# Optimization experiments

Hardware: AMD Instinct MI355X
Metric: run time of the kernel (lower is better)

The kernel has to match this reference:

```python
import jax, jax.numpy as jnp
import numpy as np

INIT_RANGE = 0.02

def setup_inputs() -> dict:
    key = jax.random.key(0)
    ks = jax.random.split(key, 5)
    B, S, D, H, Dh = 4, 2048, 768, 12, 64
    residual = jax.random.normal(ks[0], (B, S, D), dtype=jnp.float32)
    W_Q = jax.random.normal(ks[1], (H, D, Dh), dtype=jnp.float32) * INIT_RANGE
    W_K = jax.random.normal(ks[2], (H, D, Dh), dtype=jnp.float32) * INIT_RANGE
    W_V = jax.random.normal(ks[3], (H, D, Dh), dtype=jnp.float32) * INIT_RANGE
    W_O = jax.random.normal(ks[4], (H, Dh, D), dtype=jnp.float32) * INIT_RANGE
    b_Q = jnp.zeros((H, Dh), dtype=jnp.float32)
    b_K = jnp.zeros((H, Dh), dtype=jnp.float32)
    b_V = jnp.zeros((H, Dh), dtype=jnp.float32)
    b_O = jnp.zeros((D,), dtype=jnp.float32)
    return {"residual": residual, "W_Q": W_Q, "W_K": W_K, "W_V": W_V,
            "W_O": W_O, "b_Q": b_Q, "b_K": b_K, "b_V": b_V, "b_O": b_O}

def reference(residual, W_Q, W_K, W_V, W_O, b_Q, b_K, b_V, b_O):
    # residual: [b, s, d]; W_{Q,K,V}: [h, d, dh]; W_O: [h, dh, d]
    d_head = W_Q.shape[-1]
    q = jnp.einsum('bsd,hde->bshe', residual, W_Q) + b_Q  # [b, s, h, dh]
    k = jnp.einsum('bsd,hde->bshe', residual, W_K) + b_K
    v = jnp.einsum('bsd,hde->bshe', residual, W_V) + b_V
    scores = jnp.einsum('bqhe,bkhe->bhqk', q, k) / jnp.sqrt(jnp.float32(d_head))
    S = residual.shape[1]
    causal = jnp.tril(jnp.ones((S, S), dtype=bool))  # True where attending allowed
    scores = jnp.where(causal, scores, -jnp.inf)
    pattern = jax.nn.softmax(scores, axis=-1)  # [b, h, q, k]
    z = jnp.einsum('bkhe,bhqk->bqhe', v, pattern)  # [b, q, h, dh]
    attn_out = jnp.einsum('bqhe,hed->bqd', z, W_O) + b_O
    return attn_out
```

## Files before the change

kernel.cpp:

```cpp
#include <hip/hip_runtime.h>

typedef short short8 __attribute__((ext_vector_type(8)));
typedef float floatx4 __attribute__((ext_vector_type(4)));
typedef unsigned short ushort_t;


__device__ inline ushort_t f2bf(float f) {
  union { float f; unsigned u; } x; x.f = f;
  unsigned u = x.u;
  unsigned r = u + 0x7fffu + ((u >> 16) & 1u);
  return (ushort_t)(r >> 16);
}

__device__ inline unsigned pk2(float a, float b) {
  union { float f; unsigned u; } x, y; x.f = a; y.f = b;
  return ((x.u + 0x8000u) >> 16) | ((y.u + 0x8000u) & 0xffff0000u);
}

__device__ inline float fexp2(float x) {
#if __has_builtin(__builtin_amdgcn_exp2f)
  return __builtin_amdgcn_exp2f(x);
#else
  return exp2f(x);
#endif
}

__device__ inline void async16(const void* g, void* l) {
  __builtin_amdgcn_global_load_lds((const __attribute__((address_space(1))) void*)g,
                                   (__attribute__((address_space(3))) void*)l,
                                   16, 0, 0);
}


__global__ __launch_bounds__(256) void conv_prep(
    const float* __restrict__ x, ushort_t* __restrict__ rx,
    const float* __restrict__ wq, const float* __restrict__ wk, const float* __restrict__ wv,
    const float* __restrict__ wo,
    const float* __restrict__ bq, const float* __restrict__ bk, const float* __restrict__ bv,
    ushort_t* __restrict__ wqkvT, ushort_t* __restrict__ woT, float* __restrict__ bqkv)
{
  __shared__ ushort_t t[64 * 72];
  const int tid = threadIdx.x;
  const int bid0 = blockIdx.x;
  if (bid0 < 6144) {
    int i = bid0 * 256 + tid;
    float4 f = ((const float4*)x)[i];
    ushort4 o;
    o.x = f2bf(f.x); o.y = f2bf(f.y); o.z = f2bf(f.z); o.w = f2bf(f.w);
    ((ushort4*)rx)[i] = o;
    return;
  }
  const int bid = bid0 - 6144;
  if (bid < 432) {
    int m = bid / 144, rem = bid % 144;
    int h = rem / 12, dt = rem % 12;
    int d0 = dt * 64;
    const float* w = (m == 0) ? wq : ((m == 1) ? wk : wv);
    const float* src = w + ((size_t)h * 768 + d0) * 64;
#pragma unroll
    for (int i = 0; i < 4; ++i) {
      int task = i * 256 + tid;
      int row = task >> 4, c4 = task & 15;
      float4 f = *(const float4*)(src + row * 64 + c4 * 4);
      ushort4 o4;
      o4.x = f2bf(f.x); o4.y = f2bf(f.y); o4.z = f2bf(f.z); o4.w = f2bf(f.w);
      *(ushort4*)&t[row * 72 + c4 * 4] = o4;
    }
    __syncthreads();
    ushort_t* dst = wqkvT + ((size_t)m * 768 + h * 64) * 768 + d0;
#pragma unroll
    for (int i = 0; i < 2; ++i) {
      int task = i * 256 + tid;
      int e = task >> 3, sc = task & 7;
      short8 d8;
#pragma unroll
      for (int j = 0; j < 8; ++j) d8[j] = (short)t[(sc * 8 + j) * 72 + e];
      *(short8*)(dst + (size_t)e * 768 + sc * 8) = d8;
    }
  } else if (bid < 576) {
    int b2 = bid - 432;
    int het = b2 / 12, dt = b2 % 12;
    int he0 = het * 64, d0 = dt * 64;
    const float* src = wo + (size_t)he0 * 768 + d0;
#pragma unroll
    for (int i = 0; i < 4; ++i) {
      int task = i * 256 + tid;
      int row = task >> 4, c4 = task & 15;
      float4 f = *(const float4*)(src + (size_t)row * 768 + c4 * 4);
      ushort4 o4;
      o4.x = f2bf(f.x); o4.y = f2bf(f.y); o4.z = f2bf(f.z); o4.w = f2bf(f.w);
      *(ushort4*)&t[row * 72 + c4 * 4] = o4;
    }
    __syncthreads();
    ushort_t* dst = woT + (size_t)d0 * 768 + he0;
#pragma unroll
    for (int i = 0; i < 2; ++i) {
      int task = i * 256 + tid;
      int dd = task >> 3, sc = task & 7;
      short8 d8;
#pragma unroll
      for (int j = 0; j < 8; ++j) d8[j] = (short)t[(sc * 8 + j) * 72 + dd];
      *(short8*)(dst + (size_t)dd * 768 + sc * 8) = d8;
    }
  } else {
    for (int idx = tid; idx < 2304; idx += 256) {
      int m = idx / 768, rem = idx - m * 768;
      const float* bp = (m == 0) ? bq : ((m == 1) ? bk : bv);
      bqkv[idx] = bp[rem];
    }
  }
}


__global__ __launch_bounds__(256) void gemm_qkv(
    const ushort_t* __restrict__ A, const ushort_t* __restrict__ Bt,
    const float* __restrict__ bias,
    ushort_t* __restrict__ q, ushort_t* __restrict__ k, ushort_t* __restrict__ vt)
{
  __shared__ ushort_t sh[17408];
  const int tid = threadIdx.x;
  const int wave = tid >> 6, lane = tid & 63;
  const int ln15 = lane & 15, quad = lane >> 4;
  const int id = blockIdx.x;
  const int xk = id & 7, j = id >> 3;
  const int bx = (xk >> 1) * 16 + (j & 15);
  const int by = (xk & 1) * 9 + (j >> 4);
  const int row0 = bx * 128, col0 = by * 128;
  const int wm = (wave >> 1) * 64, wn = (wave & 1) * 64;
  const int c0 = wave * 2;

  const ushort_t* gA0 = A + (size_t)(row0 + c0 * 16 + (lane >> 2)) * 768 + (lane & 3) * 8;
  const ushort_t* gB0 = Bt + (size_t)(col0 + c0 * 16 + (lane >> 2)) * 768 + (lane & 3) * 8;

  floatx4 acc[4][4];
#pragma unroll
  for (int mi = 0; mi < 4; ++mi)
#pragma unroll
    for (int ni = 0; ni < 4; ++ni)
      acc[mi][ni] = (floatx4){0.f, 0.f, 0.f, 0.f};

  async16(gA0, &sh[c0 * 512]);
  async16(gA0 + 16 * 768, &sh[c0 * 512 + 512]);
  async16(gB0, &sh[8192 + c0 * 512]);
  async16(gB0 + 16 * 768, &sh[8192 + c0 * 512 + 512]);
  __syncthreads();

  for (int kt = 0; kt < 24; ++kt) {
    const int buf = kt & 1;
    if (kt + 1 < 24) {
      ushort_t* dA = &sh[(buf ^ 1) * 4096];
      ushort_t* dB = &sh[8192 + (buf ^ 1) * 4096];
      async16(gA0 + (kt + 1) * 32, dA + c0 * 512);
      async16(gA0 + (kt + 1) * 32 + 16 * 768, dA + c0 * 512 + 512);
      async16(gB0 + (kt + 1) * 32, dB + c0 * 512);
      async16(gB0 + (kt + 1) * 32 + 16 * 768, dB + c0 * 512 + 512);
    }
    const ushort_t* sA = &sh[buf * 4096];
    const ushort_t* sB = &sh[8192 + buf * 4096];
    short8 af[4], bfv[4];
#pragma unroll
    for (int mi = 0; mi < 4; ++mi)
      af[mi] = *(const short8*)&sA[(wm + mi * 16 + ln15) * 32 + quad * 8];
#pragma unroll
    for (int ni = 0; ni < 4; ++ni)
      bfv[ni] = *(const short8*)&sB[(wn + ni * 16 + ln15) * 32 + quad * 8];
#pragma unroll
    for (int mi = 0; mi < 4; ++mi)
#pragma unroll
      for (int ni = 0; ni < 4; ++ni)
        acc[mi][ni] = __builtin_amdgcn_mfma_f32_16x16x32_bf16(af[mi], bfv[ni], acc[mi][ni], 0, 0, 0);
    __syncthreads();
  }

  if (col0 < 1536) {
    const float qscale = 0.125f * 1.44269504f;
#pragma unroll
    for (int mi = 0; mi < 4; ++mi) {
#pragma unroll
      for (int ni = 0; ni < 4; ++ni) {
        int gr = row0 + wm + mi * 16 + quad * 4;
        int gc = col0 + wn + ni * 16 + ln15;
        float bia = bias[gc];
        int m = gc >> 9 >> 1;
        m = gc / 768;
        int rem = gc - m * 768;
        int h = rem >> 6, e = rem & 63;
        ushort_t* dp = (m == 0) ? q : k;
#pragma unroll
        for (int r = 0; r < 4; ++r) {
          float val = acc[mi][ni][r] + bia;
          int rr = gr + r;
          int bb = rr >> 11, ss = rr & 2047;
          size_t dst = ((size_t)((bb * 12 + h) * 2048 + ss) << 6) + e;
          dp[dst] = f2bf((m == 0) ? val * qscale : val);
        }
      }
    }
  } else {
#pragma unroll
    for (int mi = 0; mi < 4; ++mi) {
#pragma unroll
      for (int ni = 0; ni < 4; ++ni) {
        int col = wn + ni * 16 + ln15;
        int rowb = wm + mi * 16 + quad * 4;
        float bia = bias[col0 + col];
        ushort4 w4;
        w4.x = f2bf(acc[mi][ni][0] + bia);
        w4.y = f2bf(acc[mi][ni][1] + bia);
        w4.z = f2bf(acc[mi][ni][2] + bia);
        w4.w = f2bf(acc[mi][ni][3] + bia);
        *(ushort4*)&sh[col * 136 + rowb] = w4;
      }
    }
    __syncthreads();
    const int relc0 = col0 - 1536;
    const int bb = row0 >> 11, s0 = row0 & 2047;
#pragma unroll
    for (int i = 0; i < 8; ++i) {
      int g = i * 256 + tid;
      int col = g >> 4, chunk = g & 15;
      short8 d = *(const short8*)&sh[col * 136 + chunk * 8];
      int hh = (relc0 + col) >> 6;
      int ee = col & 63;
      *(short8*)(vt + (((size_t)(bb * 12 + hh) * 64 + ee) << 11) + s0 + chunk * 8) = d;
    }
  }
}


__global__ __launch_bounds__(256) void gemm_out(
    const ushort_t* __restrict__ A, const ushort_t* __restrict__ Bt,
    const float* __restrict__ bias, float* __restrict__ outf)
{
  __shared__ ushort_t lA[2][64 * 32];
  __shared__ ushort_t lB[2][128 * 32];
  const int tid = threadIdx.x;
  const int wave = tid >> 6, lane = tid & 63;
  const int ln15 = lane & 15, quad = lane >> 4;
  const int id = blockIdx.x;
  const int xk = id & 7, j = id >> 3;
  const int bx = xk * 16 + (j & 15);
  const int by = j >> 4;
  const int row0 = bx * 64, col0 = by * 128;
  const int wm = (wave >> 1) * 32, wn = (wave & 1) * 64;
  const int cb = wave * 2;

  const ushort_t* gA0 = A + (size_t)(row0 + wave * 16 + (lane >> 2)) * 768 + (lane & 3) * 8;
  const ushort_t* gB0 = Bt + (size_t)(col0 + cb * 16 + (lane >> 2)) * 768 + (lane & 3) * 8;

  floatx4 acc[2][4];
#pragma unroll
  for (int mi = 0; mi < 2; ++mi)
#pragma unroll
    for (int ni = 0; ni < 4; ++ni)
      acc[mi][ni] = (floatx4){0.f, 0.f, 0.f, 0.f};

  async16(gA0, &lA[0][wave * 512]);
  async16(gB0, &lB[0][cb * 512]);
  async16(gB0 + 16 * 768, &lB[0][cb * 512 + 512]);
  __syncthreads();

  for (int kt = 0; kt < 24; ++kt) {
    const int buf = kt & 1;
    if (kt + 1 < 24) {
      async16(gA0 + (kt + 1) * 32, &lA[buf ^ 1][wave * 512]);
      async16(gB0 + (kt + 1) * 32, &lB[buf ^ 1][cb * 512]);
      async16(gB0 + (kt + 1) * 32 + 16 * 768, &lB[buf ^ 1][cb * 512 + 512]);
    }
    short8 af[2], bfv[4];
#pragma unroll
    for (int mi = 0; mi < 2; ++mi)
      af[mi] = *(const short8*)&lA[buf][(wm + mi * 16 + ln15) * 32 + quad * 8];
#pragma unroll
    for (int ni = 0; ni < 4; ++ni)
      bfv[ni] = *(const short8*)&lB[buf][(wn + ni * 16 + ln15) * 32 + quad * 8];
#pragma unroll
    for (int mi = 0; mi < 2; ++mi)
#pragma unroll
      for (int ni = 0; ni < 4; ++ni)
        acc[mi][ni] = __builtin_amdgcn_mfma_f32_16x16x32_bf16(af[mi], bfv[ni], acc[mi][ni], 0, 0, 0);
    __syncthreads();
  }

#pragma unroll
  for (int mi = 0; mi < 2; ++mi) {
#pragma unroll
    for (int ni = 0; ni < 4; ++ni) {
      int gr = row0 + wm + mi * 16 + quad * 4;
      int gc = col0 + wn + ni * 16 + ln15;
      float bia = bias[gc];
#pragma unroll
      for (int r = 0; r < 4; ++r)
        outf[(size_t)(gr + r) * 768 + gc] = acc[mi][ni][r] + bia;
    }
  }
}


__device__ inline short8 frag_ld(const ushort_t* t, int row, int ch) {
  return *(const short8*)&t[row * 64 + (((ch ^ row) & 7) * 8)];
}

__global__ __launch_bounds__(256) void attn3(
    const ushort_t* __restrict__ Q, const ushort_t* __restrict__ K,
    const ushort_t* __restrict__ VT, ushort_t* __restrict__ Z)
{
  __shared__ ushort_t lK[2][64 * 64];
  __shared__ ushort_t lV[2][64 * 64];
  __shared__ ushort_t lPQ[128 * 64];
  const int tid = threadIdx.x;
  const int wave = tid >> 6, lane = tid & 63;
  const int ln15 = lane & 15, quad = lane >> 4;
  const int bi = blockIdx.x;
  const int bh = bi % 48;
  const int t = 15 - (bi / 48);
  const int h = bh % 12, b = bh / 12;
  const size_t base = (size_t)bh * 2048 * 64;
  const ushort_t* Qp = Q + base + (size_t)t * 128 * 64;
  const ushort_t* Kp = K + base;
  const ushort_t* Vp = VT + base;
  const int nk = 2 * t + 2;

  const int srow = tid >> 3, slch = tid & 7;
  const int sc_ = slch ^ (srow & 7);

#pragma unroll
  for (int i = 0; i < 4; ++i) {
    int task = i * 256 + tid;
    int row = task >> 3;
    int c = slch ^ (row & 7);
    async16(Qp + row * 64 + c * 8, &lPQ[task * 8]);
  }
  async16(Kp + (size_t)srow * 64 + sc_ * 8, &lK[0][tid * 8]);
  async16(Kp + (size_t)(srow + 32) * 64 + sc_ * 8, &lK[0][(256 + tid) * 8]);
  async16(Vp + (size_t)srow * 2048 + sc_ * 8, &lV[0][tid * 8]);
  async16(Vp + (size_t)(srow + 32) * 2048 + sc_ * 8, &lV[0][(256 + tid) * 8]);

  const ushort_t* kPre0 = Kp + (size_t)(64 + srow) * 64 + sc_ * 8;
  const ushort_t* kPre1 = kPre0 + 32 * 64;
  const ushort_t* vPre0 = Vp + (size_t)srow * 2048 + 64 + sc_ * 8;
  const ushort_t* vPre1 = vPre0 + 32 * 2048;

  __syncthreads();
  short8 qf[2][2];
#pragma unroll
  for (int c = 0; c < 2; ++c) {
    qf[c][0] = frag_ld(lPQ, wave * 32 + c * 16 + ln15, quad);
    qf[c][1] = frag_ld(lPQ, wave * 32 + c * 16 + ln15, quad + 4);
  }
  __syncthreads();

  float l_i[2] = {0.f, 0.f};
  floatx4 o[2][4];
#pragma unroll
  for (int c = 0; c < 2; ++c)
#pragma unroll
    for (int et = 0; et < 4; ++et) o[c][et] = (floatx4){0.f, 0.f, 0.f, 0.f};

  ushort_t* lPw = lPQ + wave * 2048;
  const int qg0 = t * 128 + wave * 32 + ln15;

  for (int kt = 0; kt < nk; ++kt) {
    const int buf = kt & 1;
    if (kt + 1 < nk) {
      ushort_t* dK = lK[buf ^ 1];
      ushort_t* dV = lV[buf ^ 1];
      async16(kPre0, dK + tid * 8);
      async16(kPre1, dK + (256 + tid) * 8);
      async16(vPre0, dV + tid * 8);
      async16(vPre1, dV + (256 + tid) * 8);
      kPre0 += 4096; kPre1 += 4096; vPre0 += 64; vPre1 += 64;
    }

    floatx4 st[2][4];
#pragma unroll
    for (int ni = 0; ni < 4; ++ni) {
      short8 kf0 = frag_ld(lK[buf], ni * 16 + ln15, quad);
      short8 kf1 = frag_ld(lK[buf], ni * 16 + ln15, quad + 4);
#pragma unroll
      for (int c = 0; c < 2; ++c) {
        floatx4 z4 = (floatx4){0.f, 0.f, 0.f, 0.f};
        z4 = __builtin_amdgcn_mfma_f32_16x16x32_bf16(kf0, qf[c][0], z4, 0, 0, 0);
        st[c][ni] = __builtin_amdgcn_mfma_f32_16x16x32_bf16(kf1, qf[c][1], z4, 0, 0, 0);
      }
    }

    const bool masked = (kt >= 2 * t);
#pragma unroll
    for (int c = 0; c < 2; ++c) {
      const int qg = qg0 + c * 16;
      float p[16];
      float rs = 0.f;
#pragma unroll
      for (int ni = 0; ni < 4; ++ni)
#pragma unroll
        for (int r = 0; r < 4; ++r) {
          float x = st[c][ni][r];
          if (masked) {
            int kg = kt * 64 + ni * 16 + quad * 4 + r;
            x = (kg <= qg) ? x : -1e30f;
          }
          float pe = fexp2(x);
          p[ni * 4 + r] = pe;
          rs += pe;
        }
      rs += __shfl_xor(rs, 16);
      rs += __shfl_xor(rs, 32);
      l_i[c] += rs;
      const int rowl = c * 16 + ln15;
#pragma unroll
      for (int ni = 0; ni < 4; ++ni) {
        int chunk = 2 * ni + (quad >> 1);
        int pos = chunk ^ (rowl & 7);
        uint2 w;
        w.x = pk2(p[ni * 4 + 0], p[ni * 4 + 1]);
        w.y = pk2(p[ni * 4 + 2], p[ni * 4 + 3]);
        *(uint2*)&lPw[rowl * 64 + pos * 8 + (quad & 1) * 4] = w;
      }
    }

    short8 pf[2][2];
#pragma unroll
    for (int c = 0; c < 2; ++c) {
      pf[c][0] = frag_ld(lPw, c * 16 + ln15, quad);
      pf[c][1] = frag_ld(lPw, c * 16 + ln15, quad + 4);
    }
#pragma unroll
    for (int et = 0; et < 4; ++et) {
      short8 vf0 = frag_ld(lV[buf], et * 16 + ln15, quad);
      short8 vf1 = frag_ld(lV[buf], et * 16 + ln15, quad + 4);
#pragma unroll
      for (int c = 0; c < 2; ++c) {
        o[c][et] = __builtin_amdgcn_mfma_f32_16x16x32_bf16(vf0, pf[c][0], o[c][et], 0, 0, 0);
        o[c][et] = __builtin_amdgcn_mfma_f32_16x16x32_bf16(vf1, pf[c][1], o[c][et], 0, 0, 0);
      }
    }
    __syncthreads();
  }

#pragma unroll
  for (int c = 0; c < 2; ++c) {
    float inv = 1.f / l_i[c];
    size_t zrow = (size_t)(b * 2048 + t * 128 + wave * 32 + c * 16 + ln15);
#pragma unroll
    for (int et = 0; et < 4; ++et) {
      ushort4 w;
      w.x = f2bf(o[c][et][0] * inv);
      w.y = f2bf(o[c][et][1] * inv);
      w.z = f2bf(o[c][et][2] * inv);
      w.w = f2bf(o[c][et][3] * inv);
      *(ushort4*)&Z[zrow * 768 + h * 64 + et * 16 + quad * 4] = w;
    }
  }
}


extern "C" void kernel_launch(void* const* d_in, const int* in_sizes, int n_in,
                              void* d_out, int out_size, void* d_ws, size_t ws_size,
                              hipStream_t stream)
{
  const float* residual = (const float*)d_in[0];
  const float* W_Q = (const float*)d_in[1];
  const float* W_K = (const float*)d_in[2];
  const float* W_V = (const float*)d_in[3];
  const float* W_O = (const float*)d_in[4];
  const float* b_Q = (const float*)d_in[5];
  const float* b_K = (const float*)d_in[6];
  const float* b_V = (const float*)d_in[7];
  const float* b_O = (const float*)d_in[8];
  float* out = (float*)d_out;

  char* w = (char*)d_ws;
  ushort_t* rx    = (ushort_t*)(w + 0);
  ushort_t* wqkvT = (ushort_t*)(w + 12582912);
  ushort_t* woT   = (ushort_t*)(w + 16121856);
  float*    bqkv  = (float*)   (w + 17301504);
  ushort_t* q     = (ushort_t*)(w + 17310720);
  ushort_t* k     = (ushort_t*)(w + 29893632);
  ushort_t* vt    = (ushort_t*)(w + 55059456);
  ushort_t* z     = rx;

  conv_prep<<<6721, 256, 0, stream>>>(residual, rx, W_Q, W_K, W_V, W_O,
                                      b_Q, b_K, b_V, wqkvT, woT, bqkv);
  gemm_qkv<<<1152, 256, 0, stream>>>(rx, wqkvT, bqkv, q, k, vt);
  attn3<<<768, 256, 0, stream>>>(q, k, vt, z);
  gemm_out<<<768, 256, 0, stream>>>(z, woT, b_O, out);
}
```

Measured before the change: 220.0 us.

## Vectorize GEMM epilogues, shrink QKV LDS, skip fully-masked attention tiles

Swaps the MFMA operand order in the Q/K part of the QKV GEMM and in the output GEMM, so each lane holds four consecutive columns and can write them as ushort4 or float4, with the bias read as float4. The V transpose goes through LDS in two 64-column halves, which cuts LDS to 32 KB, and a launch-bounds hint of 5 blocks is added to raise occupancy. In attention, waves 0-1 skip the last KV tile, which lies fully above the causal diagonal for their rows. pk2 now uses a byte-permute builtin. These target scattered scalar stores, LDS-limited occupancy and wasted masked work, at the cost of an extra barrier in the V path and possible register pressure from the occupancy hint.

New measurement: 359.2 us. 1.63x slower.

```diff
diff --git a/kernel.cpp b/kernel.cpp
--- a/kernel.cpp
+++ b/kernel.cpp
@@ -14,7 +14,7 @@
 
 __device__ inline unsigned pk2(float a, float b) {
   union { float f; unsigned u; } x, y; x.f = a; y.f = b;
-  return ((x.u + 0x8000u) >> 16) | ((y.u + 0x8000u) & 0xffff0000u);
+  return __builtin_amdgcn_perm(y.u + 0x8000u, x.u + 0x8000u, 0x07060302u);
 }
 
 __device__ inline float fexp2(float x) {
@@ -112,12 +112,12 @@
 }
 
 
-__global__ __launch_bounds__(256) void gemm_qkv(
+__global__ __launch_bounds__(256, 5) void gemm_qkv(
     const ushort_t* __restrict__ A, const ushort_t* __restrict__ Bt,
     const float* __restrict__ bias,
     ushort_t* __restrict__ q, ushort_t* __restrict__ k, ushort_t* __restrict__ vt)
 {
-  __shared__ ushort_t sh[17408];
+  __shared__ ushort_t sh[16384];
   const int tid = threadIdx.x;
   const int wave = tid >> 6, lane = tid & 63;
   const int ln15 = lane & 15, quad = lane >> 4;
@@ -128,6 +128,7 @@
   const int row0 = bx * 128, col0 = by * 128;
   const int wm = (wave >> 1) * 64, wn = (wave & 1) * 64;
   const int c0 = wave * 2;
+  const bool is_v = (col0 >= 1536);
 
   const ushort_t* gA0 = A + (size_t)(row0 + c0 * 16 + (lane >> 2)) * 768 + (lane & 3) * 8;
   const ushort_t* gB0 = Bt + (size_t)(col0 + c0 * 16 + (lane >> 2)) * 768 + (lane & 3) * 8;
@@ -145,84 +146,115 @@
   async16(gB0 + 16 * 768, &sh[8192 + c0 * 512 + 512]);
   __syncthreads();
 
-  for (int kt = 0; kt < 24; ++kt) {
-    const int buf = kt & 1;
-    if (kt + 1 < 24) {
-      ushort_t* dA = &sh[(buf ^ 1) * 4096];
-      ushort_t* dB = &sh[8192 + (buf ^ 1) * 4096];
-      async16(gA0 + (kt + 1) * 32, dA + c0 * 512);
-      async16(gA0 + (kt + 1) * 32 + 16 * 768, dA + c0 * 512 + 512);
-      async16(gB0 + (kt + 1) * 32, dB + c0 * 512);
-      async16(gB0 + (kt + 1) * 32 + 16 * 768, dB + c0 * 512 + 512);
-    }
-    const ushort_t* sA = &sh[buf * 4096];
-    const ushort_t* sB = &sh[8192 + buf * 4096];
-    short8 af[4], bfv[4];
-#pragma unroll
-    for (int mi = 0; mi < 4; ++mi)
-      af[mi] = *(const short8*)&sA[(wm + mi * 16 + ln15) * 32 + quad * 8];
-#pragma unroll
-    for (int ni = 0; ni < 4; ++ni)
-      bfv[ni] = *(const short8*)&sB[(wn + ni * 16 + ln15) * 32 + quad * 8];
-#pragma unroll
-    for (int mi = 0; mi < 4; ++mi)
+  if (!is_v) {
+    for (int kt = 0; kt < 24; ++kt) {
+      const int buf = kt & 1;
+      if (kt + 1 < 24) {
+        ushort_t* dA = &sh[(buf ^ 1) * 4096];
+        ushort_t* dB = &sh[8192 + (buf ^ 1) * 4096];
+        async16(gA0 + (kt + 1) * 32, dA + c0 * 512);
+        async16(gA0 + (kt + 1) * 32 + 16 * 768, dA + c0 * 512 + 512);
+        async16(gB0 + (kt + 1) * 32, dB + c0 * 512);
+        async16(gB0 + (kt + 1) * 32 + 16 * 768, dB + c0 * 512 + 512);
+      }
+      const ushort_t* sA = &sh[buf * 4096];
+      const ushort_t* sB = &sh[8192 + buf * 4096];
+      short8 af[4], bfv[4];
+#pragma unroll
+      for (int mi = 0; mi < 4; ++mi)
+        af[mi] = *(const short8*)&sA[(wm + mi * 16 + ln15) * 32 + quad * 8];
 #pragma unroll
       for (int ni = 0; ni < 4; ++ni)
-        acc[mi][ni] = __builtin_amdgcn_mfma_f32_16x16x32_bf16(af[mi], bfv[ni], acc[mi][ni], 0, 0, 0);
-    __syncthreads();
-  }
-
-  if (col0 < 1536) {
+        bfv[ni] = *(const short8*)&sB[(wn + ni * 16 + ln15) * 32 + quad * 8];
+#pragma unroll
+      for (int mi = 0; mi < 4; ++mi)
+#pragma unroll
+        for (int ni = 0; ni < 4; ++ni)
+          acc[mi][ni] = __builtin_amdgcn_mfma_f32_16x16x32_bf16(bfv[ni], af[mi], acc[mi][ni], 0, 0, 0);
+      __syncthreads();
+    }
     const float qscale = 0.125f * 1.44269504f;
 #pragma unroll
     for (int mi = 0; mi < 4; ++mi) {
+      int rr = row0 + wm + mi * 16 + ln15;
+      int bb = rr >> 11, ss = rr & 2047;
 #pragma unroll
       for (int ni = 0; ni < 4; ++ni) {
-        int gr = row0 + wm + mi * 16 + quad * 4;
-        int gc = col0 + wn + ni * 16 + ln15;
-        float bia = bias[gc];
-        int m = gc >> 9 >> 1;
-        m = gc / 768;
-        int rem = gc - m * 768;
-        int h = rem >> 6, e = rem & 63;
-        ushort_t* dp = (m == 0) ? q : k;
-#pragma unroll
-        for (int r = 0; r < 4; ++r) {
-          float val = acc[mi][ni][r] + bia;
-          int rr = gr + r;
-          int bb = rr >> 11, ss = rr & 2047;
-          size_t dst = ((size_t)((bb * 12 + h) * 2048 + ss) << 6) + e;
-          dp[dst] = f2bf((m == 0) ? val * qscale : val);
-        }
+        int gc0 = col0 + wn + ni * 16 + quad * 4;
+        int m = (gc0 >= 768) ? 1 : 0;
+        int rem = gc0 - m * 768;
+        int h = rem >> 6, e0 = rem & 63;
+        float4 b4 = *(const float4*)&bias[gc0];
+        float sc = m ? 1.f : qscale;
+        ushort_t* dp = m ? k : q;
+        ushort4 w4;
+        w4.x = f2bf((acc[mi][ni][0] + b4.x) * sc);
+        w4.y = f2bf((acc[mi][ni][1] + b4.y) * sc);
+        w4.z = f2bf((acc[mi][ni][2] + b4.z) * sc);
+        w4.w = f2bf((acc[mi][ni][3] + b4.w) * sc);
+        *(ushort4*)(dp + (((size_t)(bb * 12 + h) * 2048 + ss) << 6) + e0) = w4;
       }
     }
   } else {
-#pragma unroll
-    for (int mi = 0; mi < 4; ++mi) {
-#pragma unroll
-      for (int ni = 0; ni < 4; ++ni) {
-        int col = wn + ni * 16 + ln15;
-        int rowb = wm + mi * 16 + quad * 4;
-        float bia = bias[col0 + col];
-        ushort4 w4;
-        w4.x = f2bf(acc[mi][ni][0] + bia);
-        w4.y = f2bf(acc[mi][ni][1] + bia);
-        w4.z = f2bf(acc[mi][ni][2] + bia);
-        w4.w = f2bf(acc[mi][ni][3] + bia);
-        *(ushort4*)&sh[col * 136 + rowb] = w4;
-      }
-    }
-    __syncthreads();
+    for (int kt = 0; kt < 24; ++kt) {
+      const int buf = kt & 1;
+      if (kt + 1 < 24) {
+        ushort_t* dA = &sh[(buf ^ 1) * 4096];
+        ushort_t* dB = &sh[8192 + (buf ^ 1) * 4096];
+        async16(gA0 + (kt + 1) * 32, dA + c0 * 512);
+        async16(gA0 + (kt + 1) * 32 + 16 * 768, dA + c0 * 512 + 512);
+        async16(gB0 + (kt + 1) * 32, dB + c0 * 512);
+        async16(gB0 + (kt + 1) * 32 + 16 * 768, dB + c0 * 512 + 512);
+      }
+      const ushort_t* sA = &sh[buf * 4096];
+      const ushort_t* sB = &sh[8192 + buf * 4096];
+      short8 af[4], bfv[4];
+#pragma unroll
+      for (int mi = 0; mi < 4; ++mi)
+        af[mi] = *(const short8*)&sA[(wm + mi * 16 + ln15) * 32 + quad * 8];
+#pragma unroll
+      for (int ni = 0; ni < 4; ++ni)
+        bfv[ni] = *(const short8*)&sB[(wn + ni * 16 + ln15) * 32 + quad * 8];
+#pragma unroll
+      for (int mi = 0; mi < 4; ++mi)
+#pragma unroll
+        for (int ni = 0; ni < 4; ++ni)
+          acc[mi][ni] = __builtin_amdgcn_mfma_f32_16x16x32_bf16(af[mi], bfv[ni], acc[mi][ni], 0, 0, 0);
+      __syncthreads();
+    }
     const int relc0 = col0 - 1536;
     const int bb = row0 >> 11, s0 = row0 & 2047;
-#pragma unroll
-    for (int i = 0; i < 8; ++i) {
-      int g = i * 256 + tid;
-      int col = g >> 4, chunk = g & 15;
-      short8 d = *(const short8*)&sh[col * 136 + chunk * 8];
-      int hh = (relc0 + col) >> 6;
-      int ee = col & 63;
-      *(short8*)(vt + (((size_t)(bb * 12 + hh) * 64 + ee) << 11) + s0 + chunk * 8) = d;
+    const int myhalf = wn >> 6;
+#pragma unroll
+    for (int hf = 0; hf < 2; ++hf) {
+      if (myhalf == hf) {
+#pragma unroll
+        for (int mi = 0; mi < 4; ++mi) {
+#pragma unroll
+          for (int ni = 0; ni < 4; ++ni) {
+            int col = wn + ni * 16 + ln15;
+            int rowb = wm + mi * 16 + quad * 4;
+            float bia = bias[col0 + col];
+            ushort4 w4;
+            w4.x = f2bf(acc[mi][ni][0] + bia);
+            w4.y = f2bf(acc[mi][ni][1] + bia);
+            w4.z = f2bf(acc[mi][ni][2] + bia);
+            w4.w = f2bf(acc[mi][ni][3] + bia);
+            *(ushort4*)&sh[(col & 63) * 136 + rowb] = w4;
+          }
+        }
+      }
+      __syncthreads();
+#pragma unroll
+      for (int i = 0; i < 4; ++i) {
+        int g = i * 256 + tid;
+        int lc = g >> 4, chunk = g & 15;
+        short8 d = *(const short8*)&sh[lc * 136 + chunk * 8];
+        int c = hf * 64 + lc;
+        int hh = (relc0 + c) >> 6, ee = (relc0 + c) & 63;
+        *(short8*)(vt + (((size_t)(bb * 12 + hh) * 64 + ee) << 11) + s0 + chunk * 8) = d;
+      }
+      if (hf == 0) __syncthreads();
     }
   }
 }
@@ -278,20 +310,23 @@
     for (int mi = 0; mi < 2; ++mi)
 #pragma unroll
       for (int ni = 0; ni < 4; ++ni)
-        acc[mi][ni] = __builtin_amdgcn_mfma_f32_16x16x32_bf16(af[mi], bfv[ni], acc[mi][ni], 0, 0, 0);
+        acc[mi][ni] = __builtin_amdgcn_mfma_f32_16x16x32_bf16(bfv[ni], af[mi], acc[mi][ni], 0, 0, 0);
     __syncthreads();
   }
 
 #pragma unroll
   for (int mi = 0; mi < 2; ++mi) {
+    int gr = row0 + wm + mi * 16 + ln15;
 #pragma unroll
     for (int ni = 0; ni < 4; ++ni) {
-      int gr = row0 + wm + mi * 16 + quad * 4;
-      int gc = col0 + wn + ni * 16 + ln15;
-      float bia = bias[gc];
-#pragma unroll
-      for (int r = 0; r < 4; ++r)
-        outf[(size_t)(gr + r) * 768 + gc] = acc[mi][ni][r] + bia;
+      int gc0 = col0 + wn + ni * 16 + quad * 4;
+      float4 b4 = *(const float4*)&bias[gc0];
+      float4 w4;
+      w4.x = acc[mi][ni][0] + b4.x;
+      w4.y = acc[mi][ni][1] + b4.y;
+      w4.z = acc[mi][ni][2] + b4.z;
+      w4.w = acc[mi][ni][3] + b4.w;
+      *(float4*)&outf[(size_t)gr * 768 + gc0] = w4;
     }
   }
 }
@@ -372,67 +407,70 @@
       kPre0 += 4096; kPre1 += 4096; vPre0 += 64; vPre1 += 64;
     }
 
-    floatx4 st[2][4];
-#pragma unroll
-    for (int ni = 0; ni < 4; ++ni) {
-      short8 kf0 = frag_ld(lK[buf], ni * 16 + ln15, quad);
-      short8 kf1 = frag_ld(lK[buf], ni * 16 + ln15, quad + 4);
+    const bool skip = (kt == nk - 1) && (wave < 2);
+    if (!skip) {
+      floatx4 st[2][4];
+#pragma unroll
+      for (int ni = 0; ni < 4; ++ni) {
+        short8 kf0 = frag_ld(lK[buf], ni * 16 + ln15, quad);
+        short8 kf1 = frag_ld(lK[buf], ni * 16 + ln15, quad + 4);
+#pragma unroll
+        for (int c = 0; c < 2; ++c) {
+          floatx4 z4 = (floatx4){0.f, 0.f, 0.f, 0.f};
+          z4 = __builtin_amdgcn_mfma_f32_16x16x32_bf16(kf0, qf[c][0], z4, 0, 0, 0);
+          st[c][ni] = __builtin_amdgcn_mfma_f32_16x16x32_bf16(kf1, qf[c][1], z4, 0, 0, 0);
+        }
+      }
+
+      const bool masked = (kt >= 2 * t);
 #pragma unroll
       for (int c = 0; c < 2; ++c) {
-        floatx4 z4 = (floatx4){0.f, 0.f, 0.f, 0.f};
-        z4 = __builtin_amdgcn_mfma_f32_16x16x32_bf16(kf0, qf[c][0], z4, 0, 0, 0);
-        st[c][ni] = __builtin_amdgcn_mfma_f32_16x16x32_bf16(kf1, qf[c][1], z4, 0, 0, 0);
-      }
-    }
-
-    const bool masked = (kt >= 2 * t);
-#pragma unroll
-    for (int c = 0; c < 2; ++c) {
-      const int qg = qg0 + c * 16;
-      float p[16];
-      float rs = 0.f;
-#pragma unroll
-      for (int ni = 0; ni < 4; ++ni)
-#pragma unroll
-        for (int r = 0; r < 4; ++r) {
-          float x = st[c][ni][r];
-          if (masked) {
-            int kg = kt * 64 + ni * 16 + quad * 4 + r;
-            x = (kg <= qg) ? x : -1e30f;
+        const int qg = qg0 + c * 16;
+        float p[16];
+        float rs = 0.f;
+#pragma unroll
+        for (int ni = 0; ni < 4; ++ni)
+#pragma unroll
+          for (int r = 0; r < 4; ++r) {
+            float x = st[c][ni][r];
+            if (masked) {
+              int kg = kt * 64 + ni * 16 + quad * 4 + r;
+              x = (kg <= qg) ? x : -1e30f;
+            }
+            float pe = fexp2(x);
+            p[ni * 4 + r] = pe;
+            rs += pe;
           }
-          float pe = fexp2(x);
-          p[ni * 4 + r] = pe;
-          rs += pe;
+        rs += __shfl_xor(rs, 16);
+        rs += __shfl_xor(rs, 32);
+        l_i[c] += rs;
+        const int rowl = c * 16 + ln15;
+#pragma unroll
+        for (int ni = 0; ni < 4; ++ni) {
+          int chunk = 2 * ni + (quad >> 1);
+          int pos = chunk ^ (rowl & 7);
+          uint2 w;
+          w.x = pk2(p[ni * 4 + 0], p[ni * 4 + 1]);
+          w.y = pk2(p[ni * 4 + 2], p[ni * 4 + 3]);
+          *(uint2*)&lPw[rowl * 64 + pos * 8 + (quad & 1) * 4] = w;
         }
-      rs += __shfl_xor(rs, 16);
-      rs += __shfl_xor(rs, 32);
-      l_i[c] += rs;
-      const int rowl = c * 16 + ln15;
-#pragma unroll
-      for (int ni = 0; ni < 4; ++ni) {
-        int chunk = 2 * ni + (quad >> 1);
-        int pos = chunk ^ (rowl & 7);
-        uint2 w;
-        w.x = pk2(p[ni * 4 + 0], p[ni * 4 + 1]);
-        w.y = pk2(p[ni * 4 + 2], p[ni * 4 + 3]);
-        *(uint2*)&lPw[rowl * 64 + pos * 8 + (quad & 1) * 4] = w;
-      }
-    }
-
-    short8 pf[2][2];
-#pragma unroll
-    for (int c = 0; c < 2; ++c) {
-      pf[c][0] = frag_ld(lPw, c * 16 + ln15, quad);
-      pf[c][1] = frag_ld(lPw, c * 16 + ln15, quad + 4);
-    }
-#pragma unroll
-    for (int et = 0; et < 4; ++et) {
-      short8 vf0 = frag_ld(lV[buf], et * 16 + ln15, quad);
-      short8 vf1 = frag_ld(lV[buf], et * 16 + ln15, quad + 4);
+      }
+
+      short8 pf[2][2];
 #pragma unroll
       for (int c = 0; c < 2; ++c) {
-        o[c][et] = __builtin_amdgcn_mfma_f32_16x16x32_bf16(vf0, pf[c][0], o[c][et], 0, 0, 0);
-        o[c][et] = __builtin_amdgcn_mfma_f32_16x16x32_bf16(vf1, pf[c][1], o[c][et], 0, 0, 0);
+        pf[c][0] = frag_ld(lPw, c * 16 + ln15, quad);
+        pf[c][1] = frag_ld(lPw, c * 16 + ln15, quad + 4);
+      }
+#pragma unroll
+      for (int et = 0; et < 4; ++et) {
+        short8 vf0 = frag_ld(lV[buf], et * 16 + ln15, quad);
+        short8 vf1 = frag_ld(lV[buf], et * 16 + ln15, quad + 4);
+#pragma unroll
+        for (int c = 0; c < 2; ++c) {
+          o[c][et] = __builtin_amdgcn_mfma_f32_16x16x32_bf16(vf0, pf[c][0], o[c][et], 0, 0, 0);
+          o[c][et] = __builtin_amdgcn_mfma_f32_16x16x32_bf16(vf1, pf[c][1], o[c][et], 0, 0, 0);
+        }
       }
     }
     __syncthreads();
```
